# Kernel optimization log

Hardware: AMD Instinct MI355X
Metric: run time of the kernel (lower is better)

The kernel has to match this reference:

```python
import jax, jax.numpy as jnp
import numpy as np

B, H, W, DIM = 16, 28, 28, 256
HEADS, K = 8, 7
HD = DIM // HEADS
MLP = int(DIM * 4.0)
EPS = 1e-5


def setup_inputs() -> dict:
    key = jax.random.key(0)
    ks = jax.random.split(key, 8)
    s = 0.02
    return {
        "x": jax.random.normal(ks[0], (B, H, W, DIM), jnp.float32),
        "norm1_w": jnp.ones((DIM,), jnp.float32),
        "norm1_b": jnp.zeros((DIM,), jnp.float32),
        "qkv_w": jax.random.normal(ks[1], (3 * DIM, DIM), jnp.float32) * s,
        "qkv_b": jnp.zeros((3 * DIM,), jnp.float32),
        "rpb": jax.random.normal(ks[2], (HEADS, 2 * K - 1, 2 * K - 1), jnp.float32) * s,
        "proj_w": jax.random.normal(ks[3], (DIM, DIM), jnp.float32) * s,
        "proj_b": jnp.zeros((DIM,), jnp.float32),
        "norm2_w": jnp.ones((DIM,), jnp.float32),
        "norm2_b": jnp.zeros((DIM,), jnp.float32),
        "fc1_w": jax.random.normal(ks[4], (MLP, DIM), jnp.float32) * s,
        "fc1_b": jnp.zeros((MLP,), jnp.float32),
        "fc2_w": jax.random.normal(ks[5], (DIM, MLP), jnp.float32) * s,
        "fc2_b": jnp.zeros((DIM,), jnp.float32),
    }


def _ln(x, w, b):
    m = jnp.mean(x, axis=-1, keepdims=True)
    v = jnp.var(x, axis=-1, keepdims=True)  # biased, as torch LayerNorm
    return (x - m) * jax.lax.rsqrt(v + EPS) * w + b


def _window_idx(n):
    # NATTEN border handling: window shifts so every query has exactly K neighbors
    start = jnp.clip(jnp.arange(n) - K // 2, 0, n - K)  # [n]
    idx = start[:, None] + jnp.arange(K)                # [n, K] absolute neighbor index
    rel = idx - jnp.arange(n)[:, None] + (K - 1)        # [n, K] rpb index in [0, 2K-2]
    return idx, rel


def _neighborhood_attn(x, qkv_w, qkv_b, rpb, proj_w, proj_b):
    b, h, w, c = x.shape
    qkv = (x @ qkv_w.T + qkv_b).reshape(b, h, w, 3, HEADS, HD)
    q, k, v = qkv[:, :, :, 0], qkv[:, :, :, 1], qkv[:, :, :, 2]  # [b,h,w,heads,hd]
    q = q * (HD ** -0.5)
    idx_h, rel_h = _window_idx(h)
    idx_w, rel_w = _window_idx(w)
    # gather K/V neighborhoods: [b,h,K,w,K,heads,hd]
    kwin = k[:, idx_h][:, :, :, idx_w]
    vwin = v[:, idx_h][:, :, :, idx_w]
    # logits per query (i,j) over its KxK window
    attn = jnp.einsum('bijhd,biajchd->bhijac', q, kwin)  # [b,heads,h,w,K,K]
    bias = rpb[:, rel_h]                 # [heads,h,K,2K-1]
    bias = bias[:, :, :, rel_w]          # [heads,h,K,w,K]
    bias = bias.transpose(0, 1, 3, 2, 4) # [heads,h,w,K,K]
    attn = attn + bias[None]
    attn = jax.nn.softmax(attn.reshape(b, HEADS, h, w, K * K), axis=-1)
    attn = attn.reshape(b, HEADS, h, w, K, K)
    out = jnp.einsum('bhijac,biajchd->bijhd', attn, vwin).reshape(b, h, w, c)
    return out @ proj_w.T + proj_b


def reference(x, norm1_w, norm1_b, qkv_w, qkv_b, rpb, proj_w, proj_b,
              norm2_w, norm2_b, fc1_w, fc1_b, fc2_w, fc2_b):
    shortcut = x
    x = _ln(x, norm1_w, norm1_b)
    x = shortcut + _neighborhood_attn(x, qkv_w, qkv_b, rpb, proj_w, proj_b)
    h = _ln(x, norm2_w, norm2_b) @ fc1_w.T + fc1_b
    h = jax.nn.gelu(h, approximate=False)  # torch nn.GELU default (erf)
    return x + (h @ fc2_w.T + fc2_b)
```

## Files before the change

kernel.cpp:

```cpp
#include <hip/hip_runtime.h>
#include <hip/hip_bf16.h>
#include <math.h>

#define DIM   256
#define HEADS 8
#define HD    32
#define KW    7
#define HH    28
#define WW    28
#define BBATCH 16
#define NTOK  (BBATCH*HH*WW)
#define MLPD  1024
#define EPSLN 1e-5f
#define QSCALE 0.17677669529663687f

#define AS1 __attribute__((address_space(1)))
#define AS3 __attribute__((address_space(3)))

typedef __attribute__((ext_vector_type(8))) short short8;
typedef __attribute__((ext_vector_type(4))) float f32x4;
typedef unsigned short us;

__device__ __forceinline__ float b2f(us u) {
  union { float f; unsigned u; } x; x.u = ((unsigned)u) << 16; return x.f;
}
__device__ __forceinline__ us f2b(float f) {
  union { float f; unsigned u; } x; x.f = f;
  unsigned lsb = (x.u >> 16) & 1;
  x.u += 0x7fffu + lsb;
  return (us)(x.u >> 16);
}
__device__ __forceinline__ bool probe_f32(const us* p) { return p[0] == 0; }

__device__ __forceinline__ void gll16(const us* g, us* l) {
  __builtin_amdgcn_global_load_lds((const AS1 unsigned*)(const void*)g,
                                   (AS3 unsigned*)(void*)l, 16, 0, 0);
}

__device__ __forceinline__ float gelu_f(float x) {
  const float y = 0.7978845608028654f * x * (1.0f + 0.044715f * x * x);
  const float u = __expf(2.0f * y);
  const float th = 1.0f - 2.0f / (u + 1.0f);
  return 0.5f * x * (1.0f + th);
}

__global__ __launch_bounds__(256) void pre_kernel(const void* s0, const void* s1,
                                                  const void* s2, const void* s3,
                                                  us* d0, us* d1, us* d2, us* d3,
                                                  const void* p0, const void* p1, const void* p2,
                                                  const void* p3, const void* p4, const void* p5,
                                                  const void* p6, const void* p7, const void* p8,
                                                  float* __restrict__ pack,
                                                  const void* __restrict__ x,
                                                  us* __restrict__ xn1,
                                                  us* __restrict__ bias_t,
                                                  const us* __restrict__ probe)
{
  const bool isf32 = probe_f32(probe);
  const int blk = blockIdx.x;
  const int t = threadIdx.x;
  if (blk < 768) {
    const int gi = (blk * 256 + t) * 4;
    const void* src; us* dst; int loc; bool qs = false;
    if (gi < 196608)      { src = s0; dst = d0; loc = gi; qs = (loc < 65536); }
    else if (gi < 262144) { src = s1; dst = d1; loc = gi - 196608; }
    else if (gi < 524288) { src = s2; dst = d2; loc = gi - 262144; }
    else                  { src = s3; dst = d3; loc = gi - 524288; }
    float v[4];
    if (isf32) {
      const float4 f = *(const float4*)((const float*)src + loc);
      v[0] = f.x; v[1] = f.y; v[2] = f.z; v[3] = f.w;
    } else {
      ushort4 u = *(const ushort4*)((const us*)src + loc);
      v[0] = b2f(u.x); v[1] = b2f(u.y); v[2] = b2f(u.z); v[3] = b2f(u.w);
    }
    const float sc = qs ? QSCALE : 1.0f;
    ushort4 o;
    o.x = f2b(v[0] * sc); o.y = f2b(v[1] * sc); o.z = f2b(v[2] * sc); o.w = f2b(v[3] * sc);
    *(ushort4*)(dst + loc) = o;
  } else if (blk < 777) {
    const int seg = blk - 768;
    const void* srcs[9] = {p0, p1, p2, p3, p4, p5, p6, p7, p8};
    const int offs[9] = {0, 256, 512, 1280, 1536, 1792, 2048, 3072, 3328};
    const int lens[9] = {256, 256, 768, 256, 256, 256, 1024, 256, 1352};
    const void* s = srcs[seg];
    const int off = offs[seg], len = lens[seg];
    for (int i = t; i < len; i += 256) {
      float v = isf32 ? ((const float*)s)[i] : b2f(((const us*)s)[i]);
      if (seg == 2 && i < 256) v *= QSCALE;
      pack[off + i] = v;
    }
  } else if (blk < 3913) {
    const int wave = t >> 6, lane = t & 63;
    const int tok = (blk - 777) * 4 + wave;
    const int c0 = lane * 4;
    float v[4];
    if (isf32) {
      const float4 f = *(const float4*)((const float*)x + (size_t)tok * DIM + c0);
      v[0] = f.x; v[1] = f.y; v[2] = f.z; v[3] = f.w;
    } else {
      ushort4 u = *(const ushort4*)((const us*)x + (size_t)tok * DIM + c0);
      v[0] = b2f(u.x); v[1] = b2f(u.y); v[2] = b2f(u.z); v[3] = b2f(u.w);
    }
    float s  = v[0] + v[1] + v[2] + v[3];
    float s2 = v[0]*v[0] + v[1]*v[1] + v[2]*v[2] + v[3]*v[3];
    #pragma unroll
    for (int m = 32; m; m >>= 1) { s += __shfl_xor(s, m); s2 += __shfl_xor(s2, m); }
    const float mean = s * (1.0f / DIM);
    const float var  = s2 * (1.0f / DIM) - mean * mean;
    const float rstd = rsqrtf(var + EPSLN);
    float wv[4], bv[4];
    if (isf32) {
      const float4 a = *(const float4*)((const float*)p0 + c0);
      const float4 c = *(const float4*)((const float*)p1 + c0);
      wv[0]=a.x; wv[1]=a.y; wv[2]=a.z; wv[3]=a.w;
      bv[0]=c.x; bv[1]=c.y; bv[2]=c.z; bv[3]=c.w;
    } else {
      ushort4 a = *(const ushort4*)((const us*)p0 + c0);
      ushort4 c = *(const ushort4*)((const us*)p1 + c0);
      wv[0]=b2f(a.x); wv[1]=b2f(a.y); wv[2]=b2f(a.z); wv[3]=b2f(a.w);
      bv[0]=b2f(c.x); bv[1]=b2f(c.y); bv[2]=b2f(c.z); bv[3]=b2f(c.w);
    }
    ushort4 o;
    o.x = f2b((v[0] - mean) * rstd * wv[0] + bv[0]);
    o.y = f2b((v[1] - mean) * rstd * wv[1] + bv[1]);
    o.z = f2b((v[2] - mean) * rstd * wv[2] + bv[2]);
    o.w = f2b((v[3] - mean) * rstd * wv[3] + bv[3]);
    *(ushort4*)(xn1 + (size_t)tok * DIM + c0) = o;
  } else {
    const int ph = blk - 3913;
    const int p  = ph >> 3, h = ph & 7;
    const int i0 = 2 * p;
    const int si0 = min(max(i0 - 3, 0), 21);
    us* bt = bias_t + (size_t)ph * (224 * 64);
    for (int e = 0; e < 56; ++e) {
      const int idx = e * 256 + t;
      const int kv = idx >> 6;
      const int q  = idx & 63;
      const int isub = q >> 5;
      const int cq = q & 31;
      const int iq = i0 + isub;
      const int siq = min(max(iq - 3, 0), 21);
      const int sj  = min(max(cq - 3, 0), 21);
      const int rr  = (kv * 2341) >> 16;
      const int ar  = si0 + rr;
      const int ck  = kv - rr * 28;
      const int dr = ar - siq, dc = ck - sj;
      const bool valid = (cq < 28) && (dr >= 0) && (dr < 7) && (dc >= 0) && (dc < 7);
      float val = -1e30f;
      if (valid) {
        const int ridx = h * 169 + (ar - iq + 6) * 13 + (ck - cq + 6);
        val = isf32 ? ((const float*)p8)[ridx] : b2f(((const us*)p8)[ridx]);
      }
      bt[idx] = f2b(val);
    }
  }
}

__global__ __launch_bounds__(256) void ln_kernel(const us* __restrict__ in,
                                                 const float* __restrict__ w,
                                                 const float* __restrict__ b,
                                                 us* __restrict__ out)
{
  const int t = threadIdx.x;
  const int wave = t >> 6, lane = t & 63;
  const int tok = blockIdx.x * 4 + wave;
  const int c0 = lane * 4;
  ushort4 u = *(const ushort4*)(in + (size_t)tok * DIM + c0);
  float v[4] = {b2f(u.x), b2f(u.y), b2f(u.z), b2f(u.w)};
  float s  = v[0] + v[1] + v[2] + v[3];
  float s2 = v[0]*v[0] + v[1]*v[1] + v[2]*v[2] + v[3]*v[3];
  #pragma unroll
  for (int m = 32; m; m >>= 1) { s += __shfl_xor(s, m); s2 += __shfl_xor(s2, m); }
  const float mean = s * (1.0f / DIM);
  const float var  = s2 * (1.0f / DIM) - mean * mean;
  const float rstd = rsqrtf(var + EPSLN);
  const float4 wv = *(const float4*)(w + c0);
  const float4 bv = *(const float4*)(b + c0);
  ushort4 o;
  o.x = f2b((v[0] - mean) * rstd * wv.x + bv.x);
  o.y = f2b((v[1] - mean) * rstd * wv.y + bv.y);
  o.z = f2b((v[2] - mean) * rstd * wv.z + bv.z);
  o.w = f2b((v[3] - mean) * rstd * wv.w + bv.w);
  *(ushort4*)(out + (size_t)tok * DIM + c0) = o;
}

template<int BM, int BK, int MODE>
__global__ __launch_bounds__(256) void gemm_kernel(const us* __restrict__ A,
                                                   const us* __restrict__ W,
                                                   const float* __restrict__ bias,
                                                   const void* __restrict__ resid,
                                                   void* __restrict__ out,
                                                   int N, int K,
                                                   const us* __restrict__ probe)
{
  constexpr int BN = 64;
  constexpr int MF = BM / 32;
  constexpr int NF = 2;
  constexpr int CPR = BK / 8;
  constexpr int ACH = BM * CPR;
  constexpr int BCH = BN * CPR;
  constexpr int ASZ = BM * BK;
  constexpr int BSZ = BN * BK;
  constexpr int TILEB = 2 * (ASZ + BSZ) * 2;
  constexpr int CSB = BM * BN * 4;
  constexpr int SMB = TILEB > CSB ? TILEB : CSB;
  __shared__ char smem[SMB];
  us* Asb = (us*)smem;
  us* Bsb = (us*)smem + 2 * ASZ;

  const int t = threadIdx.x;
  const int wave = t >> 6, lane = t & 63;
  const int wm = wave >> 1, wn = wave & 1;
  const int m0 = blockIdx.x * BM;
  const int n0 = blockIdx.y * BN;
  const int lm = lane & 15;
  const int g  = lane >> 4;

  const int NS = K / BK;

  #define STAGE(buf, kk)                                                         \
    {                                                                            \
      _Pragma("unroll")                                                          \
      for (int i = 0; i < ACH / 256; ++i) {                                      \
        const int slot = i * 256 + t;                                            \
        const int gc = slot ^ ((slot >> 3) & 7);                                 \
        gll16(A + (size_t)(m0 + gc / CPR) * K + (kk) + (gc % CPR) * 8,           \
              &Asb[(buf) * ASZ + slot * 8]);                                     \
      }                                                                          \
      _Pragma("unroll")                                                          \
      for (int i = 0; i < BCH / 256; ++i) {                                      \
        const int slot = i * 256 + t;                                            \
        const int gc = slot ^ ((slot >> 3) & 7);                                 \
        gll16(W + (size_t)(n0 + gc / CPR) * K + (kk) + (gc % CPR) * 8,           \
              &Bsb[(buf) * BSZ + slot * 8]);                                     \
      }                                                                          \
    }

  STAGE(0, 0);

  f32x4 acc[MF][NF] = {};
  int cur = 0;
  for (int s = 0; s < NS; ++s) {
    __syncthreads();
    if (s + 1 < NS) STAGE(cur ^ 1, (s + 1) * BK);
    #pragma unroll
    for (int kh = 0; kh < BK / 32; ++kh) {
      short8 a[MF], b[NF];
      #pragma unroll
      for (int mf = 0; mf < MF; ++mf) {
        const int row = wm * (BM / 2) + mf * 16 + lm;
        const int c = row * CPR + kh * 4 + g;
        const int sl = c ^ ((c >> 3) & 7);
        a[mf] = *(const short8*)(const void*)&Asb[cur * ASZ + sl * 8];
      }
      #pragma unroll
      for (int nf = 0; nf < NF; ++nf) {
        const int row = wn * 32 + nf * 16 + lm;
        const int c = row * CPR + kh * 4 + g;
        const int sl = c ^ ((c >> 3) & 7);
        b[nf] = *(const short8*)(const void*)&Bsb[cur * BSZ + sl * 8];
      }
      #pragma unroll
      for (int mf = 0; mf < MF; ++mf) {
        #pragma unroll
        for (int nf = 0; nf < NF; ++nf)
          acc[mf][nf] = __builtin_amdgcn_mfma_f32_16x16x32_bf16(a[mf], b[nf], acc[mf][nf], 0, 0, 0);
      }
    }
    cur ^= 1;
  }
  #undef STAGE

  const bool isf32 = (MODE == 1 || MODE == 3) ? probe_f32(probe) : false;
  const int col = lm;
  const int rb  = g * 4;
  __syncthreads();

  if (MODE == 3 && isf32) {
    float* Cf = (float*)smem;
    #pragma unroll
    for (int mf = 0; mf < MF; ++mf) {
      #pragma unroll
      for (int nf = 0; nf < NF; ++nf) {
        const int n_loc = wn * 32 + nf * 16 + col;
        const float bv = bias[n0 + n_loc];
        #pragma unroll
        for (int j = 0; j < 4; ++j) {
          const int m_loc = wm * (BM / 2) + mf * 16 + rb + j;
          const size_t off = (size_t)(m0 + m_loc) * N + (n0 + n_loc);
          float v = acc[mf][nf][j] + bv + b2f(((const us*)resid)[off]);
          Cf[m_loc * BN + (n_loc ^ ((m_loc & 7) << 3))] = v;
        }
      }
    }
    __syncthreads();
    constexpr int CH = BM * BN / 4;
    #pragma unroll
    for (int it = 0; it < CH / 256; ++it) {
      const int id = it * 256 + t;
      const int m = id >> 4, c = id & 15;
      const float4 val = *(const float4*)&Cf[m * BN + ((c ^ ((m & 7) << 1)) * 4)];
      *(float4*)((float*)out + (size_t)(m0 + m) * N + n0 + c * 4) = val;
    }
  } else {
    us* Cs = (us*)smem;
    #pragma unroll
    for (int mf = 0; mf < MF; ++mf) {
      #pragma unroll
      for (int nf = 0; nf < NF; ++nf) {
        const int n_loc = wn * 32 + nf * 16 + col;
        const float bv = bias[n0 + n_loc];
        #pragma unroll
        for (int j = 0; j < 4; ++j) {
          const int m_loc = wm * (BM / 2) + mf * 16 + rb + j;
          const size_t off = (size_t)(m0 + m_loc) * N + (n0 + n_loc);
          float v = acc[mf][nf][j] + bv;
          if (MODE == 1) v += isf32 ? ((const float*)resid)[off] : b2f(((const us*)resid)[off]);
          else if (MODE == 2) v = gelu_f(v);
          else if (MODE == 3) v += b2f(((const us*)resid)[off]);
          Cs[m_loc * BN + (n_loc ^ ((m_loc & 7) << 3))] = f2b(v);
        }
      }
    }
    __syncthreads();
    constexpr int CH = BM * BN / 8;
    #pragma unroll
    for (int it = 0; it < CH / 256; ++it) {
      const int id = it * 256 + t;
      const int m = id >> 3, c = id & 7;
      const uint4 val = *(const uint4*)&Cs[m * BN + (c ^ (m & 7)) * 8];
      *(uint4*)((us*)out + (size_t)(m0 + m) * N + n0 + c * 8) = val;
    }
  }
}

__global__ __launch_bounds__(256) void attn_kernel(const us* __restrict__ qkv,
                                                   const us* __restrict__ bias_t,
                                                   us* __restrict__ out)
{
  __shared__ us KP_lds[64 * 232];
  __shared__ us Vt_lds[32 * 232];

  const int raw = blockIdx.x;
  const int bid = (raw & 7) * 224 + (raw >> 3);
  const int b  = bid & 15;
  const int ph = bid >> 4;
  const int p  = ph >> 3;
  const int h  = ph & 7;
  const int i0 = 2 * p;
  const int t = threadIdx.x;
  const int wave = t >> 6, lane = t & 63;
  const int lm = lane & 15, g = lane >> 4;
  const int kb = g * 8;
  const int si0 = min(max(i0 - 3, 0), 21);
  const int si1 = min(max(i0 - 2, 0), 21);
  const int nch = (si1 + 7 - si0) * 112;

  const us* kg = qkv + ((size_t)(b * 784 + si0 * 28)) * 768 + 256 + h * 32;
  const us* vg = kg + 256;

  const int c0 = t, c1 = 256 + t, c2 = 512 + t, c3 = 768 + t;
  const bool has3 = c3 < nch;
  uint4 v0 = *(const uint4*)(const void*)(vg + (size_t)(c0 >> 2) * 768 + (c0 & 3) * 8);
  uint4 v1 = *(const uint4*)(const void*)(vg + (size_t)(c1 >> 2) * 768 + (c1 & 3) * 8);
  uint4 v2 = *(const uint4*)(const void*)(vg + (size_t)(c2 >> 2) * 768 + (c2 & 3) * 8);
  uint4 v3;
  if (has3) v3 = *(const uint4*)(const void*)(vg + (size_t)(c3 >> 2) * 768 + (c3 & 3) * 8);

  {
    int gk;
    gk = c0 ^ ((c0 >> 3) & 7); gll16(kg + (size_t)(gk >> 2) * 768 + (gk & 3) * 8, &KP_lds[c0 * 8]);
    gk = c1 ^ ((c1 >> 3) & 7); gll16(kg + (size_t)(gk >> 2) * 768 + (gk & 3) * 8, &KP_lds[c1 * 8]);
    gk = c2 ^ ((c2 >> 3) & 7); gll16(kg + (size_t)(gk >> 2) * 768 + (gk & 3) * 8, &KP_lds[c2 * 8]);
    if (has3) { gk = c3 ^ ((c3 >> 3) & 7); gll16(kg + (size_t)(gk >> 2) * 768 + (gk & 3) * 8, &KP_lds[c3 * 8]); }
  }

  if (nch == 784) {
    if (t < 112) *(uint4*)(void*)&KP_lds[(784 + t) * 8] = make_uint4(0, 0, 0, 0);
    const int ch = t & 31, slot = t >> 5;
    *(uint2*)(void*)&Vt_lds[ch * 232 + 196 + slot * 4] = make_uint2(0, 0);
  }

  {
    const unsigned uu0[4] = {v0.x, v0.y, v0.z, v0.w};
    const unsigned uu1[4] = {v1.x, v1.y, v1.z, v1.w};
    const unsigned uu2[4] = {v2.x, v2.y, v2.z, v2.w};
    #pragma unroll
    for (int e = 0; e < 4; ++e) {
      Vt_lds[((c0 & 3) * 8 + 2*e)     * 232 + (c0 >> 2)] = (us)(uu0[e] & 0xffffu);
      Vt_lds[((c0 & 3) * 8 + 2*e + 1) * 232 + (c0 >> 2)] = (us)(uu0[e] >> 16);
      Vt_lds[((c1 & 3) * 8 + 2*e)     * 232 + (c1 >> 2)] = (us)(uu1[e] & 0xffffu);
      Vt_lds[((c1 & 3) * 8 + 2*e + 1) * 232 + (c1 >> 2)] = (us)(uu1[e] >> 16);
      Vt_lds[((c2 & 3) * 8 + 2*e)     * 232 + (c2 >> 2)] = (us)(uu2[e] & 0xffffu);
      Vt_lds[((c2 & 3) * 8 + 2*e + 1) * 232 + (c2 >> 2)] = (us)(uu2[e] >> 16);
    }
    if (has3) {
      const unsigned uu3[4] = {v3.x, v3.y, v3.z, v3.w};
      #pragma unroll
      for (int e = 0; e < 4; ++e) {
        Vt_lds[((c3 & 3) * 8 + 2*e)     * 232 + (c3 >> 2)] = (us)(uu3[e] & 0xffffu);
        Vt_lds[((c3 & 3) * 8 + 2*e + 1) * 232 + (c3 >> 2)] = (us)(uu3[e] >> 16);
      }
    }
  }

  const int qcol_l = min((wave & 1) * 16 + lm, 27);
  const int iq = i0 + (wave >> 1);
  const short8 qa = *(const short8*)(const void*)(qkv + ((size_t)(b * 784 + iq * 28 + qcol_l)) * 768 + h * 32 + kb);

  __syncthreads();

  f32x4 s[14];
  #pragma unroll
  for (int n = 0; n < 14; ++n) {
    const int sl0 = (n * 16 + lm) * 4 + g;
    const int sl = sl0 ^ ((sl0 >> 3) & 7);
    const short8 kf = *(const short8*)(const void*)&KP_lds[sl * 8];
    f32x4 z = {0.f, 0.f, 0.f, 0.f};
    s[n] = __builtin_amdgcn_mfma_f32_16x16x32_bf16(qa, kf, z, 0, 0, 0);
  }

  __syncthreads();

  const us* bt = bias_t + (size_t)ph * (224 * 64);
  const int qb = wave * 16 + g * 4;
  float mx[4] = {-1e30f, -1e30f, -1e30f, -1e30f};
  #pragma unroll
  for (int n = 0; n < 14; ++n) {
    const ushort4 bb = *(const ushort4*)(const void*)&bt[(n * 16 + lm) * 64 + qb];
    const float bbf[4] = {b2f(bb.x), b2f(bb.y), b2f(bb.z), b2f(bb.w)};
    #pragma unroll
    for (int jj = 0; jj < 4; ++jj) {
      const float r = s[n][jj] + bbf[jj];
      s[n][jj] = r;
      mx[jj] = fmaxf(mx[jj], r);
    }
  }
  float sm[4];
  #pragma unroll
  for (int jj = 0; jj < 4; ++jj) {
    float m = mx[jj];
    m = fmaxf(m, __shfl_xor(m, 1)); m = fmaxf(m, __shfl_xor(m, 2));
    m = fmaxf(m, __shfl_xor(m, 4)); m = fmaxf(m, __shfl_xor(m, 8));
    float acc = 0.f;
    #pragma unroll
    for (int n = 0; n < 14; ++n) {
      const float e = __expf(s[n][jj] - m);
      acc += e;
      KP_lds[(qb + jj) * 232 + n * 16 + lm] = f2b(e);
    }
    acc += __shfl_xor(acc, 1); acc += __shfl_xor(acc, 2);
    acc += __shfl_xor(acc, 4); acc += __shfl_xor(acc, 8);
    sm[jj] = acc;
  }

  #pragma unroll
  for (int nto = 0; nto < 2; ++nto) {
    f32x4 o = {0.f, 0.f, 0.f, 0.f};
    #pragma unroll
    for (int ks = 0; ks < 7; ++ks) {
      const short8 pa = *(const short8*)(const void*)&KP_lds[(wave * 16 + lm) * 232 + ks * 32 + kb];
      const short8 vb = *(const short8*)(const void*)&Vt_lds[(nto * 16 + lm) * 232 + ks * 32 + kb];
      o = __builtin_amdgcn_mfma_f32_16x16x32_bf16(pa, vb, o, 0, 0, 0);
    }
    #pragma unroll
    for (int jj = 0; jj < 4; ++jj) {
      const int qc = (wave & 1) * 16 + g * 4 + jj;
      if (qc < 28) {
        const float inv = 1.0f / sm[jj];
        out[((size_t)(b * 784 + iq * 28 + qc)) * 256 + h * 32 + nto * 16 + lm] = f2b(o[jj] * inv);
      }
    }
  }
}

extern "C" void kernel_launch(void* const* d_in, const int* in_sizes, int n_in,
                              void* d_out, int out_size, void* d_ws, size_t ws_size,
                              hipStream_t stream)
{
  const us* probe = (const us*)d_in[1];

  char* ws = (char*)d_ws;
  us*    wqkv_c = (us*)(ws);
  us*    wproj_c= (us*)(ws + 393216);
  us*    wfc1_c = (us*)(ws + 524288);
  us*    wfc2_c = (us*)(ws + 1048576);
  float* pack   = (float*)(ws + 1572864);
  us*    bias_t = (us*)(ws + 1593344);
  us*    xn1    = (us*)(ws + 8015872);
  us*    qkv    = (us*)(ws + 14438400);
  us*    out1   = (us*)(ws + 33705984);
  us*    hbuf   = (us*)(ws + 40128512);
  us*    att    = xn1;
  us*    xn2    = qkv;

  const float* p_qkvb = pack + 512;
  const float* p_projb= pack + 1280;
  const float* p_n2w  = pack + 1536;
  const float* p_n2b  = pack + 1792;
  const float* p_fc1b = pack + 2048;
  const float* p_fc2b = pack + 3072;

  pre_kernel<<<4025, 256, 0, stream>>>(d_in[3], d_in[6], d_in[10], d_in[12],
                                       wqkv_c, wproj_c, wfc1_c, wfc2_c,
                                       d_in[1], d_in[2], d_in[4], d_in[7], d_in[8], d_in[9],
                                       d_in[11], d_in[13], d_in[5], pack,
                                       d_in[0], xn1, bias_t, probe);
  gemm_kernel<128, 32, 0><<<dim3(NTOK / 128, 768 / 64), 256, 0, stream>>>(xn1, wqkv_c, p_qkvb, nullptr, qkv, 768, 256, probe);
  attn_kernel<<<BBATCH * (HH / 2) * HEADS, 256, 0, stream>>>(qkv, bias_t, att);
  gemm_kernel<64, 64, 1><<<dim3(NTOK / 64, DIM / 64), 256, 0, stream>>>(att, wproj_c, p_projb, d_in[0], out1, DIM, 256, probe);
  ln_kernel<<<NTOK / 4, 256, 0, stream>>>(out1, p_n2w, p_n2b, xn2);
  gemm_kernel<128, 32, 2><<<dim3(NTOK / 128, MLPD / 64), 256, 0, stream>>>(xn2, wfc1_c, p_fc1b, nullptr, hbuf, MLPD, 256, probe);
  gemm_kernel<64, 64, 3><<<dim3(NTOK / 64, DIM / 64), 256, 0, stream>>>(hbuf, wfc2_c, p_fc2b, out1, d_out, DIM, MLPD, probe);
}
```

Baseline: 118.8 us.

## Precompute exp of relative bias, drop softmax max pass, widen GEMM N tiles

```diff
diff --git a/kernel.cpp b/kernel.cpp
--- a/kernel.cpp
+++ b/kernel.cpp
@@ -147,12 +147,13 @@
       const int ck  = kv - rr * 28;
       const int dr = ar - siq, dc = ck - sj;
       const bool valid = (cq < 28) && (dr >= 0) && (dr < 7) && (dc >= 0) && (dc < 7);
-      float val = -1e30f;
+      float ev = 0.f;
       if (valid) {
         const int ridx = h * 169 + (ar - iq + 6) * 13 + (ck - cq + 6);
-        val = isf32 ? ((const float*)p8)[ridx] : b2f(((const us*)p8)[ridx]);
-      }
-      bt[idx] = f2b(val);
+        const float bvv = isf32 ? ((const float*)p8)[ridx] : b2f(((const us*)p8)[ridx]);
+        ev = __expf(bvv);
+      }
+      bt[idx] = f2b(ev);
     }
   }
 }
@@ -185,7 +186,7 @@
   *(ushort4*)(out + (size_t)tok * DIM + c0) = o;
 }
 
-template<int BM, int BK, int MODE>
+template<int BM, int BN, int BK, int MODE>
 __global__ __launch_bounds__(256) void gemm_kernel(const us* __restrict__ A,
                                                    const us* __restrict__ W,
                                                    const float* __restrict__ bias,
@@ -194,16 +195,15 @@
                                                    int N, int K,
                                                    const us* __restrict__ probe)
 {
-  constexpr int BN = 64;
   constexpr int MF = BM / 32;
-  constexpr int NF = 2;
+  constexpr int NF = BN / 32;
   constexpr int CPR = BK / 8;
   constexpr int ACH = BM * CPR;
   constexpr int BCH = BN * CPR;
   constexpr int ASZ = BM * BK;
   constexpr int BSZ = BN * BK;
   constexpr int TILEB = 2 * (ASZ + BSZ) * 2;
-  constexpr int CSB = BM * BN * 4;
+  constexpr int CSB = (MODE == 3) ? BM * BN * 4 : BM * BN * 2;
   constexpr int SMB = TILEB > CSB ? TILEB : CSB;
   __shared__ char smem[SMB];
   us* Asb = (us*)smem;
@@ -256,7 +256,7 @@
       }
       #pragma unroll
       for (int nf = 0; nf < NF; ++nf) {
-        const int row = wn * 32 + nf * 16 + lm;
+        const int row = wn * (BN / 2) + nf * 16 + lm;
         const int c = row * CPR + kh * 4 + g;
         const int sl = c ^ ((c >> 3) & 7);
         b[nf] = *(const short8*)(const void*)&Bsb[cur * BSZ + sl * 8];
@@ -283,7 +283,7 @@
     for (int mf = 0; mf < MF; ++mf) {
       #pragma unroll
       for (int nf = 0; nf < NF; ++nf) {
-        const int n_loc = wn * 32 + nf * 16 + col;
+        const int n_loc = wn * (BN / 2) + nf * 16 + col;
         const float bv = bias[n0 + n_loc];
         #pragma unroll
         for (int j = 0; j < 4; ++j) {
@@ -299,7 +299,7 @@
     #pragma unroll
     for (int it = 0; it < CH / 256; ++it) {
       const int id = it * 256 + t;
-      const int m = id >> 4, c = id & 15;
+      const int m = id / (BN / 4), c = id % (BN / 4);
       const float4 val = *(const float4*)&Cf[m * BN + ((c ^ ((m & 7) << 1)) * 4)];
       *(float4*)((float*)out + (size_t)(m0 + m) * N + n0 + c * 4) = val;
     }
@@ -309,7 +309,7 @@
     for (int mf = 0; mf < MF; ++mf) {
       #pragma unroll
       for (int nf = 0; nf < NF; ++nf) {
-        const int n_loc = wn * 32 + nf * 16 + col;
+        const int n_loc = wn * (BN / 2) + nf * 16 + col;
         const float bv = bias[n0 + n_loc];
         #pragma unroll
         for (int j = 0; j < 4; ++j) {
@@ -328,7 +328,7 @@
     #pragma unroll
     for (int it = 0; it < CH / 256; ++it) {
       const int id = it * 256 + t;
-      const int m = id >> 3, c = id & 7;
+      const int m = id / (BN / 8), c = id % (BN / 8);
       const uint4 val = *(const uint4*)&Cs[m * BN + (c ^ (m & 7)) * 8];
       *(uint4*)((us*)out + (size_t)(m0 + m) * N + n0 + c * 8) = val;
     }
@@ -425,34 +425,25 @@
 
   const us* bt = bias_t + (size_t)ph * (224 * 64);
   const int qb = wave * 16 + g * 4;
-  float mx[4] = {-1e30f, -1e30f, -1e30f, -1e30f};
+  float acc4[4] = {0.f, 0.f, 0.f, 0.f};
   #pragma unroll
   for (int n = 0; n < 14; ++n) {
     const ushort4 bb = *(const ushort4*)(const void*)&bt[(n * 16 + lm) * 64 + qb];
-    const float bbf[4] = {b2f(bb.x), b2f(bb.y), b2f(bb.z), b2f(bb.w)};
+    const float eb[4] = {b2f(bb.x), b2f(bb.y), b2f(bb.z), b2f(bb.w)};
     #pragma unroll
     for (int jj = 0; jj < 4; ++jj) {
-      const float r = s[n][jj] + bbf[jj];
-      s[n][jj] = r;
-      mx[jj] = fmaxf(mx[jj], r);
+      const float e = __expf(s[n][jj]) * eb[jj];
+      acc4[jj] += e;
+      KP_lds[(qb + jj) * 232 + n * 16 + lm] = f2b(e);
     }
   }
   float sm[4];
   #pragma unroll
   for (int jj = 0; jj < 4; ++jj) {
-    float m = mx[jj];
-    m = fmaxf(m, __shfl_xor(m, 1)); m = fmaxf(m, __shfl_xor(m, 2));
-    m = fmaxf(m, __shfl_xor(m, 4)); m = fmaxf(m, __shfl_xor(m, 8));
-    float acc = 0.f;
-    #pragma unroll
-    for (int n = 0; n < 14; ++n) {
-      const float e = __expf(s[n][jj] - m);
-      acc += e;
-      KP_lds[(qb + jj) * 232 + n * 16 + lm] = f2b(e);
-    }
-    acc += __shfl_xor(acc, 1); acc += __shfl_xor(acc, 2);
-    acc += __shfl_xor(acc, 4); acc += __shfl_xor(acc, 8);
-    sm[jj] = acc;
+    float v = acc4[jj];
+    v += __shfl_xor(v, 1); v += __shfl_xor(v, 2);
+    v += __shfl_xor(v, 4); v += __shfl_xor(v, 8);
+    sm[jj] = v;
   }
 
   #pragma unroll
@@ -507,10 +498,10 @@
                                        d_in[1], d_in[2], d_in[4], d_in[7], d_in[8], d_in[9],
                                        d_in[11], d_in[13], d_in[5], pack,
                                        d_in[0], xn1, bias_t, probe);
-  gemm_kernel<128, 32, 0><<<dim3(NTOK / 128, 768 / 64), 256, 0, stream>>>(xn1, wqkv_c, p_qkvb, nullptr, qkv, 768, 256, probe);
+  gemm_kernel<128, 128, 32, 0><<<dim3(NTOK / 128, 768 / 128), 256, 0, stream>>>(xn1, wqkv_c, p_qkvb, nullptr, qkv, 768, 256, probe);
   attn_kernel<<<BBATCH * (HH / 2) * HEADS, 256, 0, stream>>>(qkv, bias_t, att);
-  gemm_kernel<64, 64, 1><<<dim3(NTOK / 64, DIM / 64), 256, 0, stream>>>(att, wproj_c, p_projb, d_in[0], out1, DIM, 256, probe);
+  gemm_kernel<64, 64, 64, 1><<<dim3(NTOK / 64, DIM / 64), 256, 0, stream>>>(att, wproj_c, p_projb, d_in[0], out1, DIM, 256, probe);
   ln_kernel<<<NTOK / 4, 256, 0, stream>>>(out1, p_n2w, p_n2b, xn2);
-  gemm_kernel<128, 32, 2><<<dim3(NTOK / 128, MLPD / 64), 256, 0, stream>>>(xn2, wfc1_c, p_fc1b, nullptr, hbuf, MLPD, 256, probe);
-  gemm_kernel<64, 64, 3><<<dim3(NTOK / 64, DIM / 64), 256, 0, stream>>>(hbuf, wfc2_c, p_fc2b, out1, d_out, DIM, MLPD, probe);
-}
+  gemm_kernel<128, 128, 32, 2><<<dim3(NTOK / 128, MLPD / 128), 256, 0, stream>>>(xn2, wfc1_c, p_fc1b, nullptr, hbuf, MLPD, 256, probe);
+  gemm_kernel<64, 64, 64, 3><<<dim3(NTOK / 64, DIM / 64), 256, 0, stream>>>(hbuf, wfc2_c, p_fc2b, out1, d_out, DIM, MLPD, probe);
+}
```

Measured after the change: 119.6 us. Within noise of the previous version (+0.7%).
